# Performance work log

Measured on AMD Instinct MI355X. Metric: run time of the kernel, lower is better.

## Reference

```python
import jax, jax.numpy as jnp
import numpy as np

N_NODES = 100000
EPS = 1e-07


def _gconv(src, dst, x, W, b):
    # DGL GraphConv with norm='both': D_dst^{-1/2} A (D_src^{-1/2} x) W + b
    ones = jnp.ones(src.shape[0], x.dtype)
    deg_out = jax.ops.segment_sum(ones, src, num_segments=N_NODES)
    deg_in = jax.ops.segment_sum(ones, dst, num_segments=N_NODES)
    norm_out = jnp.where(deg_out > 0, deg_out, 1.0) ** -0.5
    norm_in = jnp.where(deg_in > 0, deg_in, 1.0) ** -0.5
    h = x * norm_out[:, None]
    agg = jax.ops.segment_sum(h[src], dst, num_segments=N_NODES)  # [N, d]
    agg = agg * norm_in[:, None]
    return agg @ W + b


def _branch(npemb, gauss, unif, temp, Wm, bm, Wl, bl, Wq, bq, Wd1, bd1, WdX, bdX, Wc, bc):
    cat = unif.shape[-1]
    mean = npemb @ Wm + bm                      # [E, d_z]
    logstd = npemb @ Wl + bl                    # [E, d_z]
    Nlat = gauss * jnp.exp(logstd) + mean       # reparameterization
    Nlat = Nlat.reshape(npemb.shape[0], cat, -1)  # [E, cat, d_m]
    q = npemb @ Wq + bq                         # [E, cat]
    gumbel = -jnp.log(-jnp.log(unif + EPS) + EPS)
    Z = jax.nn.softmax((q + gumbel) / temp, axis=-1)  # [E, cat]
    M = jnp.einsum('ec,ecd->ed', Z, Nlat)       # [E, d_m]
    X = jax.nn.relu(jax.nn.relu(M @ Wd1 + bd1) @ WdX + bdX)
    A = jax.nn.softmax(M @ Wc + bc, axis=-1)
    return A, X, mean, logstd, q


def setup_inputs() -> dict:
    key = jax.random.key(0)
    ks = jax.random.split(key, 32)
    E_g, E = 800000, 262144
    d_in, d_h, d_z, cat, d_m, d_dec, d_out = 128, 256, 256, 4, 64, 256, 128
    s = 0.05
    inp = {
        'x': jax.random.normal(ks[0], (N_NODES, d_in), jnp.float32),
        'src': jax.random.randint(ks[1], (E_g,), 0, N_NODES),
        'dst': jax.random.randint(ks[2], (E_g,), 0, N_NODES),
        'pos_src': jax.random.randint(ks[3], (E,), 0, N_NODES),
        'pos_dst': jax.random.randint(ks[4], (E,), 0, N_NODES),
        'neg_src': jax.random.randint(ks[5], (E,), 0, N_NODES),
        'neg_dst': jax.random.randint(ks[6], (E,), 0, N_NODES),
        'gauss_pos': jax.random.normal(ks[7], (E, d_z), jnp.float32),
        'gauss_neg': jax.random.normal(ks[8], (E, d_z), jnp.float32),
        'unif_pos': jax.random.uniform(ks[9], (E, cat), jnp.float32),
        'unif_neg': jax.random.uniform(ks[10], (E, cat), jnp.float32),
        'temp': 1,
        'W1': jax.random.normal(ks[11], (d_in, d_h), jnp.float32) * s,
        'b1': jnp.zeros((d_h,), jnp.float32),
        'W2': jax.random.normal(ks[12], (d_h, d_h), jnp.float32) * s,
        'b2': jnp.zeros((d_h,), jnp.float32),
        'Wm': jax.random.normal(ks[13], (d_h, d_z), jnp.float32) * s,
        'bm': jnp.zeros((d_z,), jnp.float32),
        'Wl': jax.random.normal(ks[14], (d_h, d_z), jnp.float32) * s,
        'bl': jnp.zeros((d_z,), jnp.float32),
        'Wq': jax.random.normal(ks[15], (d_h, cat), jnp.float32) * s,
        'bq': jnp.zeros((cat,), jnp.float32),
        'Wd1': jax.random.normal(ks[16], (d_m, d_dec), jnp.float32) * s,
        'bd1': jnp.zeros((d_dec,), jnp.float32),
        'WdX': jax.random.normal(ks[17], (d_dec, d_out), jnp.float32) * s,
        'bdX': jnp.zeros((d_out,), jnp.float32),
        'Wc': jax.random.normal(ks[18], (d_m, cat), jnp.float32) * s,
        'bc': jnp.zeros((cat,), jnp.float32),
    }
    return inp


def reference(x, src, dst, pos_src, pos_dst, neg_src, neg_dst,
              gauss_pos, gauss_neg, unif_pos, unif_neg, temp,
              W1, b1, W2, b2, Wm, bm, Wl, bl, Wq, bq,
              Wd1, bd1, WdX, bdX, Wc, bc):
    # two-layer GraphConv encoder (relu after layer 0; dropout in eval mode = identity)
    h = jax.nn.relu(_gconv(src, dst, x, W1, b1))
    h = _gconv(src, dst, h, W2, b2)
    # u_add_v edge gather
    pos_npemb = h[pos_src] + h[pos_dst]
    neg_npemb = h[neg_src] + h[neg_dst]
    t = jnp.asarray(temp, h.dtype)
    posA, posX, pos_mean, pos_logstd, posq = _branch(
        pos_npemb, gauss_pos, unif_pos, t, Wm, bm, Wl, bl, Wq, bq, Wd1, bd1, WdX, bdX, Wc, bc)
    negA, negX, neg_mean, neg_logstd, negq = _branch(
        neg_npemb, gauss_neg, unif_neg, t, Wm, bm, Wl, bl, Wq, bq, Wd1, bd1, WdX, bdX, Wc, bc)
    return (posA, negA, posX, negX, pos_mean, neg_mean,
            pos_logstd, neg_logstd, posq, negq)
```

## Files before the change

kernel.cpp:

```cpp
#include <hip/hip_runtime.h>
#include <hip/hip_bf16.h>


#define NN 100000
#define EG 800000
#define EE 262144
#define NB 98

typedef __attribute__((ext_vector_type(8))) short short8;
typedef __attribute__((ext_vector_type(4))) float f32x4;
typedef __attribute__((ext_vector_type(2))) float f32x2;

__device__ __forceinline__ float lo2f(unsigned u) {
  union { unsigned u; float f; } v; v.u = u << 16; return v.f;
}
__device__ __forceinline__ float hi2f(unsigned u) {
  union { unsigned u; float f; } v; v.u = u & 0xFFFF0000u; return v.f;
}
__device__ __forceinline__ unsigned short f2bf(float f) {
  union { float f; unsigned u; } v; v.f = f;
  return (unsigned short)((v.u + 0x7FFFu + ((v.u >> 16) & 1u)) >> 16);
}
__device__ __forceinline__ unsigned pack2bf(float a, float b) {
  return (unsigned)f2bf(a) | ((unsigned)f2bf(b) << 16);
}
__device__ __forceinline__ int permc(int c) {
  return (c & ~31) | ((c & 15) << 1) | ((c >> 4) & 1);
}

__device__ __forceinline__ float decode_scalar(const void* p) {
  unsigned u = *(const unsigned*)p;
  float f = __uint_as_float(u);
  float af = fabsf(f);
  if (af >= 1e-6f && af <= 1e6f) return f;
  if (u < 1024u) return (float)u;
  return 1.0f;
}

__global__ __launch_bounds__(256) void k_deg(const int* __restrict__ src,
                                             const int* __restrict__ dst,
                                             int* __restrict__ degO,
                                             int* __restrict__ degI) {
  for (int i = blockIdx.x * 256 + threadIdx.x; i < EG; i += gridDim.x * 256) {
    atomicAdd(&degO[src[i]], 1);
    atomicAdd(&degI[dst[i]], 1);
  }
}

__global__ __launch_bounds__(1024) void k_scan1(const int* __restrict__ degI,
                                                int* __restrict__ rowptr,
                                                int* __restrict__ bsum) {
  __shared__ int wsum[16];
  int t = threadIdx.x, lane = t & 63, wv = t >> 6;
  int i = blockIdx.x * 1024 + t;
  int v = (i < NN) ? degI[i] : 0;
  int incl = v;
#pragma unroll
  for (int off = 1; off < 64; off <<= 1) {
    int u = __shfl_up(incl, off);
    if (lane >= off) incl += u;
  }
  if (lane == 63) wsum[wv] = incl;
  __syncthreads();
  if (wv == 0 && lane < 16) {
    int s = wsum[lane];
    int si = s;
#pragma unroll
    for (int off = 1; off < 16; off <<= 1) {
      int u = __shfl_up(si, off);
      if (lane >= off) si += u;
    }
    wsum[lane] = si - s;
    if (lane == 15) bsum[blockIdx.x] = si;
  }
  __syncthreads();
  int excl = wsum[wv] + incl - v;
  if (i < NN) rowptr[i] = excl;
}

__global__ __launch_bounds__(128) void k_scan2(int* __restrict__ bsum) {
  __shared__ int w0tot;
  int t = threadIdx.x, lane = t & 63, wv = t >> 6;
  int v = (t < NB) ? bsum[t] : 0;
  int incl = v;
#pragma unroll
  for (int off = 1; off < 64; off <<= 1) {
    int u = __shfl_up(incl, off);
    if (lane >= off) incl += u;
  }
  if (wv == 0 && lane == 63) w0tot = incl;
  __syncthreads();
  int excl = incl - v + (wv ? w0tot : 0);
  if (t < NB) bsum[t] = excl;
}

__global__ __launch_bounds__(1024) void k_scan3(const int* __restrict__ degI,
                                                const int* __restrict__ degO,
                                                int* __restrict__ rowptr,
                                                int* __restrict__ cursor,
                                                const int* __restrict__ bsum,
                                                float* __restrict__ normO,
                                                float* __restrict__ normI) {
  int i = blockIdx.x * 1024 + threadIdx.x;
  if (i < NN) {
    int vv = rowptr[i] + bsum[blockIdx.x];
    rowptr[i] = vv;
    cursor[i] = vv;
    if (i == NN - 1) rowptr[NN] = vv + degI[i];
    int dO = degO[i]; if (dO < 1) dO = 1;
    int dI = degI[i]; if (dI < 1) dI = 1;
    normO[i] = rsqrtf((float)dO);
    normI[i] = rsqrtf((float)dI);
  }
}

__global__ __launch_bounds__(256) void k_fill(const int* __restrict__ src,
                                              const int* __restrict__ dst,
                                              int* __restrict__ cursor,
                                              int* __restrict__ csr) {
  for (int e = blockIdx.x * 256 + threadIdx.x; e < EG; e += gridDim.x * 256) {
    int d = dst[e];
    int pos = atomicAdd(&cursor[d], 1);
    csr[pos] = src[e];
  }
}

__global__ __launch_bounds__(256) void k_transpose_all(
    const float* __restrict__ W1, const float* __restrict__ W2,
    const float* __restrict__ Wm, const float* __restrict__ Wl,
    const float* __restrict__ Wd1, const float* __restrict__ WdX,
    const float* __restrict__ Wq,
    unsigned short* __restrict__ W1T, unsigned short* __restrict__ W2T,
    unsigned short* __restrict__ WmT, unsigned short* __restrict__ WlT,
    unsigned short* __restrict__ Wd1T, unsigned short* __restrict__ WdXT,
    unsigned short* __restrict__ WqT) {
  int idx = blockIdx.x * 256 + threadIdx.x;
  if (idx < 32768) {
    int n = idx & 255, k = idx >> 8;
    W1T[n * 128 + k] = f2bf(W1[idx]);
  } else if (idx < 98304) {
    int i = idx - 32768;
    int n = i & 255, k = i >> 8;
    W2T[n * 256 + k] = f2bf(W2[i]);
  } else if (idx < 163840) {
    int i = idx - 98304;
    int n = i & 255, k = i >> 8;
    WmT[n * 256 + k] = f2bf(Wm[i]);
  } else if (idx < 229376) {
    int i = idx - 163840;
    int n = i & 255, k = i >> 8;
    WlT[n * 256 + k] = f2bf(Wl[i]);
  } else if (idx < 245760) {
    int i = idx - 229376;
    int n = i & 255, k = i >> 8;
    Wd1T[n * 64 + k] = f2bf(Wd1[i]);
  } else if (idx < 278528) {
    int i = idx - 245760;
    int n = i & 127, k = i >> 7;
    WdXT[n * 256 + k] = f2bf(WdX[i]);
  } else if (idx < 282624) {
    int i = idx - 278528;
    int r = i >> 8, k = i & 255;
    WqT[i] = (r < 4) ? f2bf(Wq[k * 4 + r]) : (unsigned short)0;
  }
}

__global__ __launch_bounds__(256) void k_gather1(
    const float* __restrict__ x, const int* __restrict__ rowptr,
    const int* __restrict__ csr, const float* __restrict__ normO,
    const float* __restrict__ normI, unsigned short* __restrict__ agg) {
  int wid = (blockIdx.x * 256 + threadIdx.x) >> 6;
  int lane = threadIdx.x & 63;
  int half = lane >> 5, fl = lane & 31;
  int nw = (gridDim.x * 256) >> 6;
  for (int n = wid; n < NN; n += nw) {
    int beg = rowptr[n], end = rowptr[n + 1];
    float a0 = 0.f, a1 = 0.f, a2 = 0.f, a3 = 0.f;
    for (int i = beg + half; i < end; i += 2) {
      int s = csr[i];
      float ns = normO[s];
      float4 v = *(const float4*)(x + ((size_t)s << 7) + (fl << 2));
      a0 += ns * v.x; a1 += ns * v.y; a2 += ns * v.z; a3 += ns * v.w;
    }
    a0 += __shfl_xor(a0, 32); a1 += __shfl_xor(a1, 32);
    a2 += __shfl_xor(a2, 32); a3 += __shfl_xor(a3, 32);
    if (lane < 32) {
      float ni = normI[n];
      *(uint2*)(agg + ((size_t)n << 7) + (fl << 2)) =
          make_uint2(pack2bf(a0 * ni, a1 * ni), pack2bf(a2 * ni, a3 * ni));
    }
  }
}

__global__ __launch_bounds__(256) void k_gather2(
    const unsigned short* __restrict__ h1s, const int* __restrict__ rowptr,
    const int* __restrict__ csr, const float* __restrict__ normI,
    unsigned short* __restrict__ agg) {
  int wid = (blockIdx.x * 256 + threadIdx.x) >> 6;
  int lane = threadIdx.x & 63;
  int half = lane >> 5, fl = lane & 31;
  int nw = (gridDim.x * 256) >> 6;
  for (int n = wid; n < NN; n += nw) {
    int beg = rowptr[n], end = rowptr[n + 1];
    float a0 = 0.f, a1 = 0.f, a2 = 0.f, a3 = 0.f, a4 = 0.f, a5 = 0.f, a6 = 0.f, a7 = 0.f;
    for (int i = beg + half; i < end; i += 2) {
      int s = csr[i];
      uint4 v = *(const uint4*)(h1s + ((size_t)s << 8) + (fl << 3));
      a0 += lo2f(v.x); a1 += hi2f(v.x);
      a2 += lo2f(v.y); a3 += hi2f(v.y);
      a4 += lo2f(v.z); a5 += hi2f(v.z);
      a6 += lo2f(v.w); a7 += hi2f(v.w);
    }
    a0 += __shfl_xor(a0, 32); a1 += __shfl_xor(a1, 32);
    a2 += __shfl_xor(a2, 32); a3 += __shfl_xor(a3, 32);
    a4 += __shfl_xor(a4, 32); a5 += __shfl_xor(a5, 32);
    a6 += __shfl_xor(a6, 32); a7 += __shfl_xor(a7, 32);
    if (lane < 32) {
      float ni = normI[n];
      uint4 o;
      o.x = pack2bf(a0 * ni, a1 * ni);
      o.y = pack2bf(a2 * ni, a3 * ni);
      o.z = pack2bf(a4 * ni, a5 * ni);
      o.w = pack2bf(a6 * ni, a7 * ni);
      *(uint4*)(agg + ((size_t)n << 8) + (fl << 3)) = o;
    }
  }
}

template <int K, bool RELU, bool OSCALE>
__global__ __launch_bounds__(256) void k_gemm(
    const unsigned short* __restrict__ A, const float* __restrict__ oscale,
    const unsigned short* __restrict__ WT, const float* __restrict__ bias,
    unsigned short* __restrict__ C, int M) {
  __shared__ __align__(16) short At[128 * 40];
  __shared__ __align__(16) short Bt[256 * 40];
  const int t = threadIdx.x;
  const int row0 = blockIdx.x * 128;
  const int lane = t & 63, wave = t >> 6;
  const int wr = (wave >> 1) << 6;
  const int wcc = (wave & 1) << 7;
  const int lrow = lane & 15, lhi = lane >> 4;

  f32x4 acc[4][8];
#pragma unroll
  for (int m = 0; m < 4; ++m)
#pragma unroll
    for (int n = 0; n < 8; ++n) acc[m][n] = (f32x4){0.f, 0.f, 0.f, 0.f};

  for (int k0 = 0; k0 < K; k0 += 32) {
    if (k0) __syncthreads();
#pragma unroll
    for (int it = 0; it < 2; ++it) {
      int idx = t + it * 256;
      int r = idx >> 2, c8 = (idx & 3) << 3;
      int grow = row0 + r;
      int4 tv = {0, 0, 0, 0};
      if (grow < M) tv = *(const int4*)(A + (size_t)grow * K + k0 + c8);
      *(int4*)&At[r * 40 + c8] = tv;
    }
    {
      const unsigned short* wt = WT + (size_t)permc(t) * K + k0;
      *(int4*)&Bt[t * 40 + 0] = *(const int4*)(wt);
      *(int4*)&Bt[t * 40 + 8] = *(const int4*)(wt + 8);
      *(int4*)&Bt[t * 40 + 16] = *(const int4*)(wt + 16);
      *(int4*)&Bt[t * 40 + 24] = *(const int4*)(wt + 24);
    }
    __syncthreads();
    short8 a[4], b[8];
#pragma unroll
    for (int m = 0; m < 4; ++m)
      a[m] = *(const short8*)&At[(wr + m * 16 + lrow) * 40 + lhi * 8];
#pragma unroll
    for (int n = 0; n < 8; ++n)
      b[n] = *(const short8*)&Bt[(wcc + n * 16 + lrow) * 40 + lhi * 8];
#pragma unroll
    for (int m = 0; m < 4; ++m)
#pragma unroll
      for (int n = 0; n < 8; ++n)
        acc[m][n] = __builtin_amdgcn_mfma_f32_16x16x32_bf16(a[m], b[n], acc[m][n], 0, 0, 0);
  }
#pragma unroll
  for (int np = 0; np < 4; ++np) {
    int tc = wcc + np * 32 + (lrow << 1);
    float bv0 = bias[tc], bv1 = bias[tc + 1];
#pragma unroll
    for (int m = 0; m < 4; ++m) {
#pragma unroll
      for (int r = 0; r < 4; ++r) {
        int grow = row0 + wr + m * 16 + lhi * 4 + r;
        if (grow < M) {
          float v0 = acc[m][2 * np][r] + bv0;
          float v1 = acc[m][2 * np + 1][r] + bv1;
          if (RELU) { v0 = fmaxf(v0, 0.f); v1 = fmaxf(v1, 0.f); }
          if (OSCALE) { float s = oscale[grow]; v0 *= s; v1 *= s; }
          *(unsigned*)&C[(size_t)grow * 256 + tc] = pack2bf(v0, v1);
        }
      }
    }
  }
}

__global__ __launch_bounds__(512) void k_branch2(
    const unsigned short* __restrict__ h, const int* __restrict__ ea,
    const int* __restrict__ eb, const float* __restrict__ gauss,
    const float* __restrict__ unif, const void* __restrict__ temp_p,
    const unsigned short* __restrict__ WmT, const float* __restrict__ bm,
    const unsigned short* __restrict__ WlT, const float* __restrict__ bl,
    const unsigned short* __restrict__ WqT, const float* __restrict__ bq,
    const float* __restrict__ Wc, const float* __restrict__ bc,
    float* __restrict__ o_mean, float* __restrict__ o_ls,
    float* __restrict__ q_o, float* __restrict__ A_o,
    unsigned* __restrict__ M_o32) {
  __shared__ __align__(16) char U[41984];
  short* At = (short*)U;
  short* Btm = (short*)(U + 8192);
  short* Btl = (short*)(U + 24576);
  short* Btq = (short*)(U + 40960);
  float* Mf = (float*)U;
  __shared__ float zS[512];
  __shared__ float qS[512];
  __shared__ float WcT[4 * 68];
  __shared__ float bmS[256], blS[256];
  __shared__ int eaS[128], ebS[128];

  const int t = threadIdx.x;
  const int e0 = blockIdx.x << 7;
  const int lane = t & 63;
  const int wv = t >> 6;
  const int lrow = lane & 15, lhi = lane >> 4;
  const int wc = wv << 5;

  if (t < 256) {
    bmS[t] = bm[t]; blS[t] = bl[t];
    WcT[(t & 3) * 68 + (t >> 2)] = Wc[t];
  } else if (t < 384) {
    eaS[t - 256] = ea[e0 + t - 256];
  } else {
    ebS[t - 384] = eb[e0 + t - 384];
  }
  __syncthreads();

  f32x4 am[8][2], al[8][2], aq;
#pragma unroll
  for (int m = 0; m < 8; ++m)
#pragma unroll
    for (int n = 0; n < 2; ++n) {
      am[m][n] = (f32x4){0.f, 0.f, 0.f, 0.f};
      al[m][n] = (f32x4){0.f, 0.f, 0.f, 0.f};
    }
  aq = (f32x4){0.f, 0.f, 0.f, 0.f};

  const int ar = t >> 2, as_ = t & 3;
  const int arsw = ((as_ ^ (ar & 3)) << 3);
  const int br = t & 255, bw = t >> 8;
  const int fsw = (lrow & 3);

  const unsigned short* pa_base = h + ((size_t)eaS[ar] << 8) + (as_ << 3);
  const unsigned short* pb_base = h + ((size_t)ebS[ar] << 8) + (as_ << 3);
  const unsigned short* wsrc_base = (bw ? WlT : WmT) + ((size_t)permc(br) << 8);
  short* bb = (bw ? Btl : Btm) + br * 32;
  const int rs = br & 3;

  uint4 va = *(const uint4*)pa_base;
  uint4 vb = *(const uint4*)pb_base;

  for (int k0 = 0; k0 < 256; k0 += 32) {
    unsigned w0 = pack2bf(lo2f(va.x) + lo2f(vb.x), hi2f(va.x) + hi2f(vb.x));
    unsigned w1 = pack2bf(lo2f(va.y) + lo2f(vb.y), hi2f(va.y) + hi2f(vb.y));
    unsigned w2 = pack2bf(lo2f(va.z) + lo2f(vb.z), hi2f(va.z) + hi2f(vb.z));
    unsigned w3 = pack2bf(lo2f(va.w) + lo2f(vb.w), hi2f(va.w) + hi2f(vb.w));
    if (k0 < 224) {
      va = *(const uint4*)(pa_base + k0 + 32);
      vb = *(const uint4*)(pb_base + k0 + 32);
    }
    if (k0) __syncthreads();
    *(int4*)&At[ar * 32 + arsw] = make_int4((int)w0, (int)w1, (int)w2, (int)w3);
    {
      const unsigned short* wsrc = wsrc_base + k0;
      *(int4*)&bb[((0 ^ rs) << 3)] = *(const int4*)(wsrc);
      *(int4*)&bb[((1 ^ rs) << 3)] = *(const int4*)(wsrc + 8);
      *(int4*)&bb[((2 ^ rs) << 3)] = *(const int4*)(wsrc + 16);
      *(int4*)&bb[((3 ^ rs) << 3)] = *(const int4*)(wsrc + 24);
    }
    if (t < 64) {
      int r = t >> 2, s = t & 3;
      *(int4*)&Btq[r * 32 + ((s ^ (r & 3)) << 3)] =
          *(const int4*)(WqT + ((size_t)r << 8) + k0 + (s << 3));
    }
    __syncthreads();
    short8 a[8], bmf[2], blf[2], bqf, aqa;
#pragma unroll
    for (int m = 0; m < 8; ++m)
      a[m] = *(const short8*)&At[(m * 16 + lrow) * 32 + ((lhi ^ fsw) << 3)];
#pragma unroll
    for (int n = 0; n < 2; ++n) {
      bmf[n] = *(const short8*)&Btm[(wc + n * 16 + lrow) * 32 + ((lhi ^ fsw) << 3)];
      blf[n] = *(const short8*)&Btl[(wc + n * 16 + lrow) * 32 + ((lhi ^ fsw) << 3)];
    }
    bqf = *(const short8*)&Btq[lrow * 32 + ((lhi ^ fsw) << 3)];
    aqa = *(const short8*)&At[((wv << 4) + lrow) * 32 + ((lhi ^ fsw) << 3)];
#pragma unroll
    for (int m = 0; m < 8; ++m)
#pragma unroll
      for (int n = 0; n < 2; ++n) {
        am[m][n] = __builtin_amdgcn_mfma_f32_16x16x32_bf16(a[m], bmf[n], am[m][n], 0, 0, 0);
        al[m][n] = __builtin_amdgcn_mfma_f32_16x16x32_bf16(a[m], blf[n], al[m][n], 0, 0, 0);
      }
    aq = __builtin_amdgcn_mfma_f32_16x16x32_bf16(aqa, bqf, aq, 0, 0, 0);
  }
  __syncthreads();

  float invt = 1.0f / decode_scalar(temp_p);
  float qb = (lrow < 4) ? bq[lrow] : 0.f;
#pragma unroll
  for (int r = 0; r < 4; ++r) {
    int el = (wv << 4) + lhi * 4 + r;
    float q = aq[r] + qb;
    float uu = 0.5f;
    if (lrow < 4) uu = unif[(((size_t)(e0 + el)) << 2) + lrow];
    float g = -__logf(-__logf(uu + 1e-7f) + 1e-7f);
    float z = (q + g) * invt;
    float mx = fmaxf(z, __shfl_xor(z, 1));
    mx = fmaxf(mx, __shfl_xor(mx, 2));
    float ez = __expf(z - mx);
    float sz = ez + __shfl_xor(ez, 1);
    sz += __shfl_xor(sz, 2);
    if (lrow < 4) { zS[el * 4 + lrow] = ez / sz; qS[el * 4 + lrow] = q; }
  }
  for (int i = t; i < 128 * 66; i += 512) Mf[i] = 0.f;
  __syncthreads();

  __builtin_nontemporal_store(qS[t], q_o + (((size_t)e0) << 2) + t);

  const int cidx = wv >> 1;
  const int dd = ((wv & 1) << 5) + (lrow << 1);
  const int tc = wc + (lrow << 1);
  float bm0 = bmS[tc], bm1 = bmS[tc + 1];
  float bl0 = blS[tc], bl1 = blS[tc + 1];
#pragma unroll
  for (int m = 0; m < 8; ++m) {
#pragma unroll
    for (int r = 0; r < 4; ++r) {
      int row = m * 16 + lhi * 4 + r;
      size_t gi = (((size_t)(e0 + row)) << 8) + tc;
      float mv0 = am[m][0][r] + bm0, mv1 = am[m][1][r] + bm1;
      float lv0 = al[m][0][r] + bl0, lv1 = al[m][1][r] + bl1;
      __builtin_nontemporal_store((f32x2){mv0, mv1}, (f32x2*)(o_mean + gi));
      __builtin_nontemporal_store((f32x2){lv0, lv1}, (f32x2*)(o_ls + gi));
      f32x2 g2 = __builtin_nontemporal_load((const f32x2*)(gauss + gi));
      float zc = zS[(row << 2) + cidx];
      atomicAdd(&Mf[row * 66 + dd], zc * (g2.x * __expf(lv0) + mv0));
      atomicAdd(&Mf[row * 66 + dd + 1], zc * (g2.y * __expf(lv1) + mv1));
    }
  }
  __syncthreads();

  {
    int e = t >> 2, cat = t & 3;
    const float* mrow = &Mf[e * 66];
    const float* wct = &WcT[cat * 68];
    float s = 0.f;
#pragma unroll
    for (int dp = 0; dp < 32; ++dp) {
      float2 m2 = *(const float2*)(mrow + 2 * dp);
      s += m2.x * wct[2 * dp] + m2.y * wct[2 * dp + 1];
    }
    s += bc[cat];
    float smx = fmaxf(s, __shfl_xor(s, 1));
    smx = fmaxf(smx, __shfl_xor(smx, 2));
    float es = __expf(s - smx);
    float ssum = es + __shfl_xor(es, 1);
    ssum += __shfl_xor(ssum, 2);
    __builtin_nontemporal_store(es / ssum, A_o + (((size_t)e0) << 2) + t);
  }
#pragma unroll
  for (int j = 0; j < 8; ++j) {
    int idx = j * 512 + t;
    int row = idx >> 5, dp = idx & 31;
    float2 m2 = *(const float2*)(&Mf[row * 66 + 2 * dp]);
    M_o32[((size_t)(e0 + row)) * 32 + dp] = pack2bf(m2.x, m2.y);
  }
}

__global__ __launch_bounds__(512) void k_dec2(
    const unsigned short* __restrict__ Mw, const unsigned short* __restrict__ Wd1T,
    const float* __restrict__ bd1, const unsigned short* __restrict__ WdXT,
    const float* __restrict__ bdX, float* __restrict__ Xo) {
  __shared__ __align__(16) char R[65280];
  short* Mt = (short*)R;
  short* Bt1 = (short*)(R + 9216);
  short* X1 = (short*)R;
  short* Bt2 = (short*)(R + 46848);
  const int t = threadIdx.x, lane = t & 63, wv = t >> 6;
  const int lrow = lane & 15, lhi = lane >> 4;
  const int e0 = blockIdx.x << 6;

  const int r2 = t >> 2, base2 = (t & 3) << 4;
  const unsigned short* wpb = WdXT + ((size_t)permc(r2) << 8) + base2;

  {
    int r = t >> 3, c8 = (t & 7) << 3;
    *(int4*)&Mt[r * 72 + c8] = *(const int4*)(Mw + (((size_t)(e0 + r)) << 6) + c8);
  }
  {
    int r1 = t >> 1, base = (t & 1) << 5;
    const unsigned short* wp = Wd1T + ((size_t)permc(r1) << 6) + base;
#pragma unroll
    for (int j = 0; j < 4; ++j)
      *(int4*)&Bt1[r1 * 72 + base + j * 8] = *(const int4*)(wp + j * 8);
  }
  int4 pw0 = *(const int4*)(wpb);
  int4 pw1 = *(const int4*)(wpb + 8);
  __syncthreads();
  f32x4 acc1[4][2];
#pragma unroll
  for (int m = 0; m < 4; ++m)
#pragma unroll
    for (int n = 0; n < 2; ++n) acc1[m][n] = (f32x4){0.f, 0.f, 0.f, 0.f};
  const int wc1 = wv << 5;
  {
    short8 a0[4], a1[4], b0[2], b1[2];
#pragma unroll
    for (int m = 0; m < 4; ++m) {
      a0[m] = *(const short8*)&Mt[(m * 16 + lrow) * 72 + lhi * 8];
      a1[m] = *(const short8*)&Mt[(m * 16 + lrow) * 72 + 32 + lhi * 8];
    }
#pragma unroll
    for (int n = 0; n < 2; ++n) {
      b0[n] = *(const short8*)&Bt1[(wc1 + n * 16 + lrow) * 72 + lhi * 8];
      b1[n] = *(const short8*)&Bt1[(wc1 + n * 16 + lrow) * 72 + 32 + lhi * 8];
    }
#pragma unroll
    for (int m = 0; m < 4; ++m)
#pragma unroll
      for (int n = 0; n < 2; ++n) {
        acc1[m][n] = __builtin_amdgcn_mfma_f32_16x16x32_bf16(a0[m], b0[n], acc1[m][n], 0, 0, 0);
        acc1[m][n] = __builtin_amdgcn_mfma_f32_16x16x32_bf16(a1[m], b1[n], acc1[m][n], 0, 0, 0);
      }
  }
  __syncthreads();
  {
    int tc = wc1 + (lrow << 1);
    float bdv0 = bd1[tc], bdv1 = bd1[tc + 1];
#pragma unroll
    for (int m = 0; m < 4; ++m)
#pragma unroll
      for (int r = 0; r < 4; ++r) {
        int row = m * 16 + lhi * 4 + r;
        float v0 = fmaxf(acc1[m][0][r] + bdv0, 0.f);
        float v1 = fmaxf(acc1[m][1][r] + bdv1, 0.f);
        *(unsigned*)&X1[row * 264 + tc] = pack2bf(v0, v1);
      }
  }

  f32x4 acc2[2][2];
#pragma unroll
  for (int m = 0; m < 2; ++m)
#pragma unroll
    for (int n = 0; n < 2; ++n) acc2[m][n] = (f32x4){0.f, 0.f, 0.f, 0.f};
  const int wr2 = (wv >> 2) << 5, wc2 = (wv & 3) << 5;
  for (int k0 = 0; k0 < 256; k0 += 64) {
    __syncthreads();
    *(int4*)&Bt2[r2 * 72 + base2] = pw0;
    *(int4*)&Bt2[r2 * 72 + base2 + 8] = pw1;
    if (k0 < 192) {
      pw0 = *(const int4*)(wpb + k0 + 64);
      pw1 = *(const int4*)(wpb + k0 + 64 + 8);
    }
    __syncthreads();
    short8 c0[2], c1[2], d0[2], d1[2];
#pragma unroll
    for (int m = 0; m < 2; ++m) {
      c0[m] = *(const short8*)&X1[(wr2 + m * 16 + lrow) * 264 + k0 + lhi * 8];
      c1[m] = *(const short8*)&X1[(wr2 + m * 16 + lrow) * 264 + k0 + 32 + lhi * 8];
    }
#pragma unroll
    for (int n = 0; n < 2; ++n) {
      d0[n] = *(const short8*)&Bt2[(wc2 + n * 16 + lrow) * 72 + lhi * 8];
      d1[n] = *(const short8*)&Bt2[(wc2 + n * 16 + lrow) * 72 + 32 + lhi * 8];
    }
#pragma unroll
    for (int m = 0; m < 2; ++m)
#pragma unroll
      for (int n = 0; n < 2; ++n) {
        acc2[m][n] = __builtin_amdgcn_mfma_f32_16x16x32_bf16(c0[m], d0[n], acc2[m][n], 0, 0, 0);
        acc2[m][n] = __builtin_amdgcn_mfma_f32_16x16x32_bf16(c1[m], d1[n], acc2[m][n], 0, 0, 0);
      }
  }
  {
    int tc2 = wc2 + (lrow << 1);
    float bx0 = bdX[tc2], bx1 = bdX[tc2 + 1];
#pragma unroll
    for (int m = 0; m < 2; ++m)
#pragma unroll
      for (int r = 0; r < 4; ++r) {
        int row = wr2 + m * 16 + lhi * 4 + r;
        float v0 = fmaxf(acc2[m][0][r] + bx0, 0.f);
        float v1 = fmaxf(acc2[m][1][r] + bx1, 0.f);
        __builtin_nontemporal_store((f32x2){v0, v1},
                                    (f32x2*)(Xo + (((size_t)(e0 + row)) << 7) + tc2));
      }
  }
}

extern "C" void kernel_launch(void* const* d_in, const int* in_sizes, int n_in,
                              void* d_out, int out_size, void* d_ws, size_t ws_size,
                              hipStream_t stream) {
  const float* x = (const float*)d_in[0];
  const int* src = (const int*)d_in[1];
  const int* dst = (const int*)d_in[2];
  const int* pos_src = (const int*)d_in[3];
  const int* pos_dst = (const int*)d_in[4];
  const int* neg_src = (const int*)d_in[5];
  const int* neg_dst = (const int*)d_in[6];
  const float* gauss_pos = (const float*)d_in[7];
  const float* gauss_neg = (const float*)d_in[8];
  const float* unif_pos = (const float*)d_in[9];
  const float* unif_neg = (const float*)d_in[10];
  const void* temp_p = d_in[11];
  const float* W1 = (const float*)d_in[12];
  const float* b1 = (const float*)d_in[13];
  const float* W2 = (const float*)d_in[14];
  const float* b2 = (const float*)d_in[15];
  const float* Wm = (const float*)d_in[16];
  const float* bm = (const float*)d_in[17];
  const float* Wl = (const float*)d_in[18];
  const float* bl = (const float*)d_in[19];
  const float* Wq = (const float*)d_in[20];
  const float* bq = (const float*)d_in[21];
  const float* Wd1 = (const float*)d_in[22];
  const float* bd1 = (const float*)d_in[23];
  const float* WdX = (const float*)d_in[24];
  const float* bdX = (const float*)d_in[25];
  const float* Wc = (const float*)d_in[26];
  const float* bc = (const float*)d_in[27];

  char* w = (char*)d_ws;
  int* degO = (int*)w;
  int* degI = (int*)(w + 401408);
  int* rowptr = (int*)(w + 802816);
  int* cursor = (int*)(w + 1204224);
  float* normO = (float*)(w + 1605632);
  float* normI = (float*)(w + 2007040);
  int* csr = (int*)(w + 2408448);
  unsigned short* W1T = (unsigned short*)(w + 5609472);
  unsigned short* W2T = (unsigned short*)(w + 5675008);
  unsigned short* WmT = (unsigned short*)(w + 5806080);
  unsigned short* WlT = (unsigned short*)(w + 5937152);
  unsigned short* Wd1T = (unsigned short*)(w + 6068224);
  unsigned short* WdXT = (unsigned short*)(w + 6100992);
  unsigned short* WqT = (unsigned short*)(w + 6166528);
  int* bsum = (int*)(w + 6174720);
  unsigned short* agg1 = (unsigned short*)(w + 6175232);
  unsigned short* h1s = (unsigned short*)(w + 31775232);
  unsigned short* agg2 = (unsigned short*)(w + 82975232);
  unsigned short* h = (unsigned short*)(w + 134175232);
  unsigned short* Mws = (unsigned short*)(w + 185375232);

  float* out = (float*)d_out;
  float* posA = out;
  float* negA = out + 1048576ull;
  float* posX = out + 2097152ull;
  float* negX = out + 35651584ull;
  float* pos_mean = out + 69206016ull;
  float* neg_mean = out + 136314880ull;
  float* pos_logstd = out + 203423744ull;
  float* neg_logstd = out + 270532608ull;
  float* posq = out + 337641472ull;
  float* negq = out + 338690048ull;

  hipMemsetAsync(d_ws, 0, 802816, stream);

  k_deg<<<1024, 256, 0, stream>>>(src, dst, degO, degI);
  k_scan1<<<NB, 1024, 0, stream>>>(degI, rowptr, bsum);
  k_scan2<<<1, 128, 0, stream>>>(bsum);
  k_scan3<<<NB, 1024, 0, stream>>>(degI, degO, rowptr, cursor, bsum, normO, normI);
  k_fill<<<1024, 256, 0, stream>>>(src, dst, cursor, csr);
  k_transpose_all<<<1104, 256, 0, stream>>>(W1, W2, Wm, Wl, Wd1, WdX, Wq,
                                            W1T, W2T, WmT, WlT, Wd1T, WdXT, WqT);

  k_gather1<<<2048, 256, 0, stream>>>(x, rowptr, csr, normO, normI, agg1);
  k_gemm<128, true, true><<<782, 256, 0, stream>>>(agg1, normO, W1T, b1, h1s, NN);
  k_gather2<<<2048, 256, 0, stream>>>(h1s, rowptr, csr, normI, agg2);
  k_gemm<256, false, false><<<782, 256, 0, stream>>>(agg2, nullptr, W2T, b2, h, NN);

  for (int b = 0; b < 2; ++b) {
    const int* es = b ? neg_src : pos_src;
    const int* ed = b ? neg_dst : pos_dst;
    const float* gs = b ? gauss_neg : gauss_pos;
    const float* uf = b ? unif_neg : unif_pos;
    float* o_mean = b ? neg_mean : pos_mean;
    float* o_ls = b ? neg_logstd : pos_logstd;
    float* o_q = b ? negq : posq;
    float* o_A = b ? negA : posA;
    float* o_X = b ? negX : posX;

    k_branch2<<<2048, 512, 0, stream>>>(h, es, ed, gs, uf, temp_p,
                                        WmT, bm, WlT, bl, WqT, bq, Wc, bc,
                                        o_mean, o_ls, o_q, o_A, (unsigned*)Mws);
    k_dec2<<<4096, 512, 0, stream>>>(Mws, Wd1T, bd1, WdXT, bdX, o_X);
  }
}
```

Baseline: 1.491 ms.

## Unroll gather loops, load branch weights directly to registers, widen fill grid

The gather kernels now unroll the neighbour loop by two with separate accumulators, so more independent loads are in flight per wavefront. In k_branch2 each wave reads its Wm/Wl/Wq B-fragments straight from global memory into registers instead of staging them through LDS. This removes the LDS stores and reads for weights and shrinks shared memory, which may raise occupancy, but it adds uncoalesced per-wave global loads of weights that every block repeats. The k_fill grid is also doubled.

```diff
diff --git a/kernel.cpp b/kernel.cpp
--- a/kernel.cpp
+++ b/kernel.cpp
@@ -176,12 +176,23 @@
   for (int n = wid; n < NN; n += nw) {
     int beg = rowptr[n], end = rowptr[n + 1];
     float a0 = 0.f, a1 = 0.f, a2 = 0.f, a3 = 0.f;
-    for (int i = beg + half; i < end; i += 2) {
-      int s = csr[i];
-      float ns = normO[s];
-      float4 v = *(const float4*)(x + ((size_t)s << 7) + (fl << 2));
-      a0 += ns * v.x; a1 += ns * v.y; a2 += ns * v.z; a3 += ns * v.w;
-    }
+    float b0 = 0.f, b1 = 0.f, b2 = 0.f, b3 = 0.f;
+    int i = beg + half;
+    for (; i + 2 < end; i += 4) {
+      int s0 = csr[i], s1 = csr[i + 2];
+      float ns0 = normO[s0], ns1 = normO[s1];
+      float4 v0 = *(const float4*)(x + ((size_t)s0 << 7) + (fl << 2));
+      float4 v1 = *(const float4*)(x + ((size_t)s1 << 7) + (fl << 2));
+      a0 += ns0 * v0.x; a1 += ns0 * v0.y; a2 += ns0 * v0.z; a3 += ns0 * v0.w;
+      b0 += ns1 * v1.x; b1 += ns1 * v1.y; b2 += ns1 * v1.z; b3 += ns1 * v1.w;
+    }
+    for (; i < end; i += 2) {
+      int s0 = csr[i];
+      float ns0 = normO[s0];
+      float4 v0 = *(const float4*)(x + ((size_t)s0 << 7) + (fl << 2));
+      a0 += ns0 * v0.x; a1 += ns0 * v0.y; a2 += ns0 * v0.z; a3 += ns0 * v0.w;
+    }
+    a0 += b0; a1 += b1; a2 += b2; a3 += b3;
     a0 += __shfl_xor(a0, 32); a1 += __shfl_xor(a1, 32);
     a2 += __shfl_xor(a2, 32); a3 += __shfl_xor(a3, 32);
     if (lane < 32) {
@@ -203,14 +214,31 @@
   for (int n = wid; n < NN; n += nw) {
     int beg = rowptr[n], end = rowptr[n + 1];
     float a0 = 0.f, a1 = 0.f, a2 = 0.f, a3 = 0.f, a4 = 0.f, a5 = 0.f, a6 = 0.f, a7 = 0.f;
-    for (int i = beg + half; i < end; i += 2) {
-      int s = csr[i];
-      uint4 v = *(const uint4*)(h1s + ((size_t)s << 8) + (fl << 3));
+    float c0 = 0.f, c1 = 0.f, c2 = 0.f, c3 = 0.f, c4 = 0.f, c5 = 0.f, c6 = 0.f, c7 = 0.f;
+    int i = beg + half;
+    for (; i + 2 < end; i += 4) {
+      int s0 = csr[i], s1 = csr[i + 2];
+      uint4 v = *(const uint4*)(h1s + ((size_t)s0 << 8) + (fl << 3));
+      uint4 u = *(const uint4*)(h1s + ((size_t)s1 << 8) + (fl << 3));
       a0 += lo2f(v.x); a1 += hi2f(v.x);
       a2 += lo2f(v.y); a3 += hi2f(v.y);
       a4 += lo2f(v.z); a5 += hi2f(v.z);
       a6 += lo2f(v.w); a7 += hi2f(v.w);
-    }
+      c0 += lo2f(u.x); c1 += hi2f(u.x);
+      c2 += lo2f(u.y); c3 += hi2f(u.y);
+      c4 += lo2f(u.z); c5 += hi2f(u.z);
+      c6 += lo2f(u.w); c7 += hi2f(u.w);
+    }
+    for (; i < end; i += 2) {
+      int s0 = csr[i];
+      uint4 v = *(const uint4*)(h1s + ((size_t)s0 << 8) + (fl << 3));
+      a0 += lo2f(v.x); a1 += hi2f(v.x);
+      a2 += lo2f(v.y); a3 += hi2f(v.y);
+      a4 += lo2f(v.z); a5 += hi2f(v.z);
+      a6 += lo2f(v.w); a7 += hi2f(v.w);
+    }
+    a0 += c0; a1 += c1; a2 += c2; a3 += c3;
+    a4 += c4; a5 += c5; a6 += c6; a7 += c7;
     a0 += __shfl_xor(a0, 32); a1 += __shfl_xor(a1, 32);
     a2 += __shfl_xor(a2, 32); a3 += __shfl_xor(a3, 32);
     a4 += __shfl_xor(a4, 32); a5 += __shfl_xor(a5, 32);
@@ -311,11 +339,8 @@
     float* __restrict__ o_mean, float* __restrict__ o_ls,
     float* __restrict__ q_o, float* __restrict__ A_o,
     unsigned* __restrict__ M_o32) {
-  __shared__ __align__(16) char U[41984];
+  __shared__ __align__(16) char U[33792];
   short* At = (short*)U;
-  short* Btm = (short*)(U + 8192);
-  short* Btl = (short*)(U + 24576);
-  short* Btq = (short*)(U + 40960);
   float* Mf = (float*)U;
   __shared__ float zS[512];
   __shared__ float qS[512];
@@ -352,14 +377,17 @@
 
   const int ar = t >> 2, as_ = t & 3;
   const int arsw = ((as_ ^ (ar & 3)) << 3);
-  const int br = t & 255, bw = t >> 8;
   const int fsw = (lrow & 3);
 
   const unsigned short* pa_base = h + ((size_t)eaS[ar] << 8) + (as_ << 3);
   const unsigned short* pb_base = h + ((size_t)ebS[ar] << 8) + (as_ << 3);
-  const unsigned short* wsrc_base = (bw ? WlT : WmT) + ((size_t)permc(br) << 8);
-  short* bb = (bw ? Btl : Btm) + br * 32;
-  const int rs = br & 3;
+  const size_t row0p = (size_t)permc(wc + lrow) << 8;
+  const size_t row1p = (size_t)permc(wc + 16 + lrow) << 8;
+  const unsigned short* bm0p = WmT + row0p + (lhi << 3);
+  const unsigned short* bm1p = WmT + row1p + (lhi << 3);
+  const unsigned short* bl0p = WlT + row0p + (lhi << 3);
+  const unsigned short* bl1p = WlT + row1p + (lhi << 3);
+  const unsigned short* bqp = WqT + ((size_t)lrow << 8) + (lhi << 3);
 
   uint4 va = *(const uint4*)pa_base;
   uint4 vb = *(const uint4*)pb_base;
@@ -373,39 +401,26 @@
       va = *(const uint4*)(pa_base + k0 + 32);
       vb = *(const uint4*)(pb_base + k0 + 32);
     }
+    short8 bmf0 = *(const short8*)(bm0p + k0);
+    short8 bmf1 = *(const short8*)(bm1p + k0);
+    short8 blf0 = *(const short8*)(bl0p + k0);
+    short8 blf1 = *(const short8*)(bl1p + k0);
+    short8 bqf = *(const short8*)(bqp + k0);
     if (k0) __syncthreads();
     *(int4*)&At[ar * 32 + arsw] = make_int4((int)w0, (int)w1, (int)w2, (int)w3);
-    {
-      const unsigned short* wsrc = wsrc_base + k0;
-      *(int4*)&bb[((0 ^ rs) << 3)] = *(const int4*)(wsrc);
-      *(int4*)&bb[((1 ^ rs) << 3)] = *(const int4*)(wsrc + 8);
-      *(int4*)&bb[((2 ^ rs) << 3)] = *(const int4*)(wsrc + 16);
-      *(int4*)&bb[((3 ^ rs) << 3)] = *(const int4*)(wsrc + 24);
-    }
-    if (t < 64) {
-      int r = t >> 2, s = t & 3;
-      *(int4*)&Btq[r * 32 + ((s ^ (r & 3)) << 3)] =
-          *(const int4*)(WqT + ((size_t)r << 8) + k0 + (s << 3));
-    }
     __syncthreads();
-    short8 a[8], bmf[2], blf[2], bqf, aqa;
+    short8 a[8], aqa;
 #pragma unroll
     for (int m = 0; m < 8; ++m)
       a[m] = *(const short8*)&At[(m * 16 + lrow) * 32 + ((lhi ^ fsw) << 3)];
-#pragma unroll
-    for (int n = 0; n < 2; ++n) {
-      bmf[n] = *(const short8*)&Btm[(wc + n * 16 + lrow) * 32 + ((lhi ^ fsw) << 3)];
-      blf[n] = *(const short8*)&Btl[(wc + n * 16 + lrow) * 32 + ((lhi ^ fsw) << 3)];
-    }
-    bqf = *(const short8*)&Btq[lrow * 32 + ((lhi ^ fsw) << 3)];
     aqa = *(const short8*)&At[((wv << 4) + lrow) * 32 + ((lhi ^ fsw) << 3)];
 #pragma unroll
-    for (int m = 0; m < 8; ++m)
-#pragma unroll
-      for (int n = 0; n < 2; ++n) {
-        am[m][n] = __builtin_amdgcn_mfma_f32_16x16x32_bf16(a[m], bmf[n], am[m][n], 0, 0, 0);
-        al[m][n] = __builtin_amdgcn_mfma_f32_16x16x32_bf16(a[m], blf[n], al[m][n], 0, 0, 0);
-      }
+    for (int m = 0; m < 8; ++m) {
+      am[m][0] = __builtin_amdgcn_mfma_f32_16x16x32_bf16(a[m], bmf0, am[m][0], 0, 0, 0);
+      am[m][1] = __builtin_amdgcn_mfma_f32_16x16x32_bf16(a[m], bmf1, am[m][1], 0, 0, 0);
+      al[m][0] = __builtin_amdgcn_mfma_f32_16x16x32_bf16(a[m], blf0, al[m][0], 0, 0, 0);
+      al[m][1] = __builtin_amdgcn_mfma_f32_16x16x32_bf16(a[m], blf1, al[m][1], 0, 0, 0);
+    }
     aq = __builtin_amdgcn_mfma_f32_16x16x32_bf16(aqa, bqf, aq, 0, 0, 0);
   }
   __syncthreads();
@@ -675,7 +690,7 @@
   k_scan1<<<NB, 1024, 0, stream>>>(degI, rowptr, bsum);
   k_scan2<<<1, 128, 0, stream>>>(bsum);
   k_scan3<<<NB, 1024, 0, stream>>>(degI, degO, rowptr, cursor, bsum, normO, normI);
-  k_fill<<<1024, 256, 0, stream>>>(src, dst, cursor, csr);
+  k_fill<<<2048, 256, 0, stream>>>(src, dst, cursor, csr);
   k_transpose_all<<<1104, 256, 0, stream>>>(W1, W2, Wm, Wl, Wd1, WdX, Wq,
                                             W1T, W2T, WmT, WlT, Wd1T, WdXT, WqT);
 
```

After: 1.375 ms. 7.8% less time.
